# Performance work log

Measured on AMD Instinct MI355X. Metric: run time of the kernel, lower is better.

## Reference

```python
import jax, jax.numpy as jnp
import numpy as np

N_NODES = 50000
N_EDGES = 600000
D = 128
H = 128


def setup_inputs() -> dict:
    key = jax.random.key(0)
    k1, k2, k3, k4 = jax.random.split(key, 4)
    x = jax.random.normal(k1, (N_NODES, D), dtype=jnp.float32)
    edge_index = jax.random.randint(k2, (2, N_EDGES), 0, N_NODES, dtype=jnp.int64)
    # Glorot-ish init for the two linear layers of SAGEConv
    scale = 1.0 / np.sqrt(D)
    W_l = jax.random.normal(k3, (H, D), dtype=jnp.float32) * scale
    b_l = jnp.zeros((H,), dtype=jnp.float32)
    W_r = jax.random.normal(k4, (H, D), dtype=jnp.float32) * scale
    return {"x": x, "edge_index": edge_index, "W_l": W_l, "b_l": b_l, "W_r": W_r}


def reference(x, edge_index, W_l, b_l, W_r):
    # PyG SAGEConv (aggr='mean', root_weight=True):
    #   out[i] = lin_l( mean_{j->i} x[j] ) + lin_r( x[i] )
    # edge_index[0] = source nodes (j), edge_index[1] = destination nodes (i)
    src = edge_index[0]
    dst = edge_index[1]
    n = x.shape[0]
    msgs = x[src]  # [E, D] gather
    agg_sum = jax.ops.segment_sum(msgs, dst, num_segments=n)  # [N, D]
    deg = jax.ops.segment_sum(jnp.ones((src.shape[0],), dtype=x.dtype), dst, num_segments=n)
    agg = agg_sum / jnp.maximum(deg, 1.0)[:, None]  # mean aggregation; 0 for isolated nodes
    out = agg @ W_l.T + b_l + x @ W_r.T  # [N, H]
    return out
```

## Files before the change

kernel.cpp:

```cpp
#include <hip/hip_runtime.h>
#include <hip/hip_bf16.h>

using f32x4 = __attribute__((ext_vector_type(4))) float;
using s16x8 = __attribute__((ext_vector_type(8))) short;

static __device__ __forceinline__ float bflo2f(unsigned int w) {
    union { unsigned int u; float f; } c; c.u = w << 16; return c.f;
}
static __device__ __forceinline__ float bfhi2f(unsigned int w) {
    union { unsigned int u; float f; } c; c.u = w & 0xffff0000u; return c.f;
}
static __device__ __forceinline__ unsigned int f2bf(float f) {
    union { float f; unsigned int u; } c; c.f = f;
    unsigned int u = c.u;
    u = u + 0x7fffu + ((u >> 16) & 1u);
    return u >> 16;
}

#define ET 8

__global__ __launch_bounds__(256) void k_convert(
        const float* __restrict__ x, unsigned short* __restrict__ xb,
        const float* __restrict__ Wr, const float* __restrict__ Wl,
        s16x8* __restrict__ wprep, int* __restrict__ bcnt, int* __restrict__ ovfn,
        int n4, int nxb)
{
    int b = blockIdx.x;
    if (b < nxb) {
        int t = b * 256 + threadIdx.x;
        if (t >= n4) return;
        float4 v = ((const float4*)x)[t];
        ushort4 o;
        o.x = (unsigned short)f2bf(v.x);
        o.y = (unsigned short)f2bf(v.y);
        o.z = (unsigned short)f2bf(v.z);
        o.w = (unsigned short)f2bf(v.w);
        ((ushort4*)xb)[t] = o;
    } else if (b < nxb + 16) {
        int s = (b - nxb) * 256 + threadIdx.x;
        if (s >= 4096) return;
        int f = s >> 6, il = s & 63;
        int nt = f >> 3, ks = f & 7;
        int col = nt * 16 + (il & 15);
        int k   = ks * 32 + (il >> 4) * 8;
        const float* Wsrc = (k < 128) ? Wr : Wl;
        int k0 = k & 127;
        const float4* wp = (const float4*)(Wsrc + (size_t)col * 128 + k0);
        float4 w0 = wp[0], w1 = wp[1];
        s16x8 v;
        v[0] = (short)f2bf(w0.x); v[1] = (short)f2bf(w0.y);
        v[2] = (short)f2bf(w0.z); v[3] = (short)f2bf(w0.w);
        v[4] = (short)f2bf(w1.x); v[5] = (short)f2bf(w1.y);
        v[6] = (short)f2bf(w1.z); v[7] = (short)f2bf(w1.w);
        wprep[s] = v;
    } else {
        int t = threadIdx.x;
        bcnt[t] = 0;
        if (t == 0) *ovfn = 0;
    }
}

__global__ __launch_bounds__(256) void k_bin(
        const int* __restrict__ src, const int* __restrict__ dst,
        int* __restrict__ bcnt, unsigned int* __restrict__ binbuf,
        int* __restrict__ ovfn, int* __restrict__ ovf,
        int E, int NB, int capb)
{
    __shared__ int hist[256];
    __shared__ int base[256];
    int t = threadIdx.x;
    hist[t] = 0;
    __syncthreads();
    int e0 = blockIdx.x * (256 * ET);
    int bins[ET], pls[ET];
    unsigned int pay[ET];
    #pragma unroll
    for (int i = 0; i < ET; ++i) {
        int e = e0 + t + i * 256;
        bins[i] = -1;
        if (e < E) {
            int d = dst[e];
            int s = src[e];
            bins[i] = d >> 8;
            pay[i]  = ((unsigned int)(d & 255) << 24) | (unsigned int)s;
            pls[i]  = atomicAdd(&hist[bins[i]], 1);
        }
    }
    __syncthreads();
    if (t < NB && hist[t] > 0) base[t] = atomicAdd(&bcnt[t], hist[t]);
    __syncthreads();
    #pragma unroll
    for (int i = 0; i < ET; ++i) {
        if (bins[i] >= 0) {
            int pos = base[bins[i]] + pls[i];
            if (pos < capb) {
                binbuf[(size_t)bins[i] * capb + pos] = pay[i];
            } else {
                int q = atomicAdd(ovfn, 1);
                ovf[2 * q]     = (bins[i] << 8) | (int)(pay[i] >> 24);
                ovf[2 * q + 1] = (int)(pay[i] & 0xFFFFFFu);
            }
        }
    }
}

__global__ __launch_bounds__(256) void k_sort(
        const int* __restrict__ bcnt, const unsigned int* __restrict__ binbuf,
        int* __restrict__ srcS, int* __restrict__ offg, int* __restrict__ degg,
        int N, int capb)
{
    __shared__ int cnt[256];
    __shared__ int sh[256];
    __shared__ int cur[256];
    int b = blockIdx.x, t = threadIdx.x;
    int m = min(bcnt[b], capb);
    cnt[t] = 0;
    __syncthreads();
    const unsigned int* bb = binbuf + (size_t)b * capb;
    for (int j = t; j < m; j += 256)
        atomicAdd(&cnt[bb[j] >> 24], 1);
    __syncthreads();
    int v = cnt[t];
    sh[t] = v;
    __syncthreads();
    #pragma unroll
    for (int d2 = 1; d2 < 256; d2 <<= 1) {
        int y = (t >= d2) ? sh[t - d2] : 0;
        __syncthreads();
        sh[t] += y;
        __syncthreads();
    }
    int off = sh[t] - v;
    cur[t] = off;
    int node = b * 256 + t;
    if (node < N) {
        offg[node] = b * capb + off;
        degg[node] = v;
    }
    __syncthreads();
    for (int j = t; j < m; j += 256) {
        unsigned int c = bb[j];
        int p = atomicAdd(&cur[c >> 24], 1);
        srcS[(size_t)b * capb + p] = (int)(c & 0xFFFFFFu);
    }
}

__global__ __launch_bounds__(256) void k_gather_wide(
        const uint4* __restrict__ xq, const int* __restrict__ srcS,
        const int* __restrict__ offg, const int* __restrict__ degg,
        const int* __restrict__ ovfn, const int* __restrict__ ovf,
        uint4* __restrict__ abq, int N)
{
    int d    = blockIdx.x * 4 + (threadIdx.x >> 6);
    int lane = threadIdx.x & 63;
    if (d >= N) return;
    int n0 = offg[d];
    int m0 = degg[d];
    const int* sl = srcS + n0;
    int c = lane & 15, r = lane >> 4;
    float a0=0,a1=0,a2=0,a3=0,a4=0,a5=0,a6=0,a7=0;
    const uint4 z4 = {0u, 0u, 0u, 0u};
    for (int p = 0; p < m0; p += 16) {
        int pe0 = p + r, pe1 = p + 4 + r, pe2 = p + 8 + r, pe3 = p + 12 + r;
        uint4 v0 = z4, v1 = z4, v2 = z4, v3 = z4;
        if (pe0 < m0) v0 = xq[(size_t)sl[pe0] * 16 + c];
        if (pe1 < m0) v1 = xq[(size_t)sl[pe1] * 16 + c];
        if (pe2 < m0) v2 = xq[(size_t)sl[pe2] * 16 + c];
        if (pe3 < m0) v3 = xq[(size_t)sl[pe3] * 16 + c];
        a0 += bflo2f(v0.x); a1 += bfhi2f(v0.x);
        a2 += bflo2f(v0.y); a3 += bfhi2f(v0.y);
        a4 += bflo2f(v0.z); a5 += bfhi2f(v0.z);
        a6 += bflo2f(v0.w); a7 += bfhi2f(v0.w);
        a0 += bflo2f(v1.x); a1 += bfhi2f(v1.x);
        a2 += bflo2f(v1.y); a3 += bfhi2f(v1.y);
        a4 += bflo2f(v1.z); a5 += bfhi2f(v1.z);
        a6 += bflo2f(v1.w); a7 += bfhi2f(v1.w);
        a0 += bflo2f(v2.x); a1 += bfhi2f(v2.x);
        a2 += bflo2f(v2.y); a3 += bfhi2f(v2.y);
        a4 += bflo2f(v2.z); a5 += bfhi2f(v2.z);
        a6 += bflo2f(v2.w); a7 += bfhi2f(v2.w);
        a0 += bflo2f(v3.x); a1 += bfhi2f(v3.x);
        a2 += bflo2f(v3.y); a3 += bfhi2f(v3.y);
        a4 += bflo2f(v3.z); a5 += bfhi2f(v3.z);
        a6 += bflo2f(v3.w); a7 += bfhi2f(v3.w);
    }
    int deg = m0;
    int nov = *ovfn;
    for (int k = 0; k < nov; ++k) {
        if (ovf[2 * k] == d) {
            ++deg;
            if (r == 0) {
                uint4 v = xq[(size_t)ovf[2 * k + 1] * 16 + c];
                a0 += bflo2f(v.x); a1 += bfhi2f(v.x);
                a2 += bflo2f(v.y); a3 += bfhi2f(v.y);
                a4 += bflo2f(v.z); a5 += bfhi2f(v.z);
                a6 += bflo2f(v.w); a7 += bfhi2f(v.w);
            }
        }
    }
    a0 += __shfl_xor(a0, 16, 64); a0 += __shfl_xor(a0, 32, 64);
    a1 += __shfl_xor(a1, 16, 64); a1 += __shfl_xor(a1, 32, 64);
    a2 += __shfl_xor(a2, 16, 64); a2 += __shfl_xor(a2, 32, 64);
    a3 += __shfl_xor(a3, 16, 64); a3 += __shfl_xor(a3, 32, 64);
    a4 += __shfl_xor(a4, 16, 64); a4 += __shfl_xor(a4, 32, 64);
    a5 += __shfl_xor(a5, 16, 64); a5 += __shfl_xor(a5, 32, 64);
    a6 += __shfl_xor(a6, 16, 64); a6 += __shfl_xor(a6, 32, 64);
    a7 += __shfl_xor(a7, 16, 64); a7 += __shfl_xor(a7, 32, 64);
    if (r == 0) {
        float inv = 1.0f / (float)max(deg, 1);
        uint4 o;
        o.x = f2bf(a0 * inv) | (f2bf(a1 * inv) << 16);
        o.y = f2bf(a2 * inv) | (f2bf(a3 * inv) << 16);
        o.z = f2bf(a4 * inv) | (f2bf(a5 * inv) << 16);
        o.w = f2bf(a6 * inv) | (f2bf(a7 * inv) << 16);
        abq[(size_t)d * 16 + c] = o;
    }
}

__global__ __launch_bounds__(256) void k_combine_mfma(
        const unsigned short* __restrict__ xb, const unsigned short* __restrict__ ab,
        const s16x8* __restrict__ wprep,
        const float* __restrict__ bl,
        float* __restrict__ out, int N, int T)
{
    __shared__ s16x8 Bf[64][64];
    int t = threadIdx.x;
    {
        const uint4* ws = (const uint4*)wprep;
        uint4* bd = (uint4*)&Bf[0][0];
        for (int s = t; s < 4096; s += 256) bd[s] = ws[s];
    }
    __syncthreads();

    int wid = t >> 6, l = t & 63;
    int lr = l & 15, lg = l >> 4;
    float bias[8];
    #pragma unroll
    for (int nt = 0; nt < 8; ++nt) bias[nt] = bl[nt * 16 + lr];

    for (int tile = blockIdx.x; tile < T; tile += gridDim.x) {
        int rb0 = tile * 128 + wid * 32;
        int rb1 = rb0 + 16;
        int ar0 = min(rb0 + lr, N - 1);
        int ar1 = min(rb1 + lr, N - 1);
        const s16x8* xr0 = (const s16x8*)(xb + (size_t)ar0 * 128);
        const s16x8* ag0 = (const s16x8*)(ab + (size_t)ar0 * 128);
        const s16x8* xr1 = (const s16x8*)(xb + (size_t)ar1 * 128);
        const s16x8* ag1 = (const s16x8*)(ab + (size_t)ar1 * 128);
        s16x8 af0[8], af1[8];
        #pragma unroll
        for (int ks = 0; ks < 4; ++ks) {
            af0[ks]     = xr0[ks * 4 + lg];
            af0[4 + ks] = ag0[ks * 4 + lg];
            af1[ks]     = xr1[ks * 4 + lg];
            af1[4 + ks] = ag1[ks * 4 + lg];
        }

        f32x4 acc0[8], acc1[8];
        #pragma unroll
        for (int nt = 0; nt < 8; ++nt) {
            float b = bias[nt];
            acc0[nt] = (f32x4){b, b, b, b};
            acc1[nt] = (f32x4){b, b, b, b};
        }

        #pragma unroll
        for (int ks = 0; ks < 8; ++ks)
            #pragma unroll
            for (int nt = 0; nt < 8; ++nt) {
                s16x8 bfrag = Bf[nt * 8 + ks][l];
                acc0[nt] = __builtin_amdgcn_mfma_f32_16x16x32_bf16(
                               af0[ks], bfrag, acc0[nt], 0, 0, 0);
                acc1[nt] = __builtin_amdgcn_mfma_f32_16x16x32_bf16(
                               af1[ks], bfrag, acc1[nt], 0, 0, 0);
            }

        #pragma unroll
        for (int i = 0; i < 4; ++i) {
            int row0 = rb0 + lg * 4 + i;
            if (row0 < N) {
                float* op = out + (size_t)row0 * 128 + lr;
                #pragma unroll
                for (int nt = 0; nt < 8; ++nt) op[nt * 16] = acc0[nt][i];
            }
            int row1 = rb1 + lg * 4 + i;
            if (row1 < N) {
                float* op = out + (size_t)row1 * 128 + lr;
                #pragma unroll
                for (int nt = 0; nt < 8; ++nt) op[nt * 16] = acc1[nt][i];
            }
        }
    }
}


__global__ __launch_bounds__(256) void k_scatter_legacy(
        const float* __restrict__ x,
        const int* __restrict__ src, const int* __restrict__ dst,
        float* __restrict__ agg, float* __restrict__ deg, int E)
{
    int e    = (int)((blockIdx.x * 256u + threadIdx.x) >> 6);
    int lane = threadIdx.x & 63;
    if (e >= E) return;
    int s = src[e];
    int d = dst[e];
    float2 v = ((const float2*)(x + (size_t)s * 128u))[lane];
    float* ar = agg + (size_t)d * 128u;
    unsafeAtomicAdd(ar + 2 * lane,     v.x);
    unsafeAtomicAdd(ar + 2 * lane + 1, v.y);
    if (lane == 0) unsafeAtomicAdd(deg + d, 1.0f);
}

__global__ __launch_bounds__(256) void k_combine_legacy(
        const float* __restrict__ x, const float* agg, const float* __restrict__ deg,
        const float* __restrict__ Wr, const float* __restrict__ Wl,
        const float* __restrict__ bl,
        float* out, int N)
{
    __shared__ uint4 WT4[64][64];
    for (int idx = threadIdx.x; idx < 64 * 64; idx += 256) {
        int g = idx >> 6, l = idx & 63;
        uint4 wv;
        unsigned int* wp = &wv.x;
        #pragma unroll
        for (int kk = 0; kk < 4; ++kk) {
            int k = g * 4 + kk;
            const float* Wsrc = (k < 128) ? Wr : Wl;
            int km = k & 127;
            unsigned int lo = f2bf(Wsrc[(size_t)l * 128 + km]);
            unsigned int hi = f2bf(Wsrc[(size_t)(l + 64) * 128 + km]);
            wp[kk] = lo | (hi << 16);
        }
        WT4[g][l] = wv;
    }
    __syncthreads();

    int wid = threadIdx.x >> 6, lane = threadIdx.x & 63;
    float b0 = bl[lane], b1 = bl[lane + 64];
    for (int row = blockIdx.x * 4 + wid; row < N; row += gridDim.x * 4) {
        const float4* xr = (const float4*)(x   + (size_t)row * 128);
        const float4* ar = (const float4*)(agg + (size_t)row * 128);
        float inv = 1.0f / fmaxf(deg[row], 1.0f);
        float acc0 = b0, acc1 = b1;
        #pragma unroll 8
        for (int c = 0; c < 32; ++c) {
            uint4 w4 = WT4[c][lane];
            float4 q = xr[c];
            #pragma unroll
            for (int j = 0; j < 4; ++j) {
                unsigned int w = (&w4.x)[j];
                float f = (&q.x)[j];
                acc0 = fmaf(f, bflo2f(w), acc0);
                acc1 = fmaf(f, bfhi2f(w), acc1);
            }
        }
        #pragma unroll 8
        for (int c = 0; c < 32; ++c) {
            uint4 w4 = WT4[c + 32][lane];
            float4 q = ar[c];
            #pragma unroll
            for (int j = 0; j < 4; ++j) {
                unsigned int w = (&w4.x)[j];
                float f = (&q.x)[j] * inv;
                acc0 = fmaf(f, bflo2f(w), acc0);
                acc1 = fmaf(f, bfhi2f(w), acc1);
            }
        }
        out[(size_t)row * 128 + lane]      = acc0;
        out[(size_t)row * 128 + lane + 64] = acc1;
    }
}


extern "C" void kernel_launch(void* const* d_in, const int* in_sizes, int n_in,
                              void* d_out, int out_size, void* d_ws, size_t ws_size,
                              hipStream_t stream)
{
    const float* x  = (const float*)d_in[0];
    const int*   ei = (const int*)d_in[1];
    const float* Wl = (const float*)d_in[2];
    const float* bl = (const float*)d_in[3];
    const float* Wr = (const float*)d_in[4];
    float*      out = (float*)d_out;

    int N = in_sizes[0] / 128;
    int E = in_sizes[1] / 2;
    const int* src = ei;
    const int* dst = ei + E;

    int NB   = (N + 255) >> 8;
    int capb = ((2 * E / (NB > 0 ? NB : 1)) + 255) & ~255;
    size_t bfB = (size_t)N * 128 * 2;

    size_t nInts = 256 + 64 + 2 * (size_t)E + 2 * (size_t)NB * capb
                 + 2 * (size_t)N;
    size_t intsB = ((nInts * 4) + 255) & ~(size_t)255;

    if (ws_size >= intsB + 2 * bfB + 65536 && NB <= 256 && N < (1 << 24)) {
        int* bcnt = (int*)d_ws;
        int* ovfn = bcnt + 256;
        int* ovf  = ovfn + 64;
        unsigned int* binbuf = (unsigned int*)(ovf + 2 * (size_t)E);
        int* srcS = (int*)(binbuf + (size_t)NB * capb);
        int* offg = srcS + (size_t)NB * capb;
        int* degg = offg + N;
        unsigned short* xb = (unsigned short*)((char*)d_ws + intsB);
        unsigned short* ab = xb + (size_t)N * 128;
        s16x8* wprep = (s16x8*)((char*)ab + bfB);

        int nxb = (N * 32 + 255) / 256;
        int ncv = nxb + 16 + 1;
        int nbin = (E + 256 * ET - 1) / (256 * ET);

        k_convert<<<ncv, 256, 0, stream>>>(x, xb, Wr, Wl, wprep, bcnt, ovfn,
                                           N * 32, nxb);
        k_bin    <<<nbin, 256, 0, stream>>>(src, dst, bcnt, binbuf, ovfn, ovf,
                                            E, NB, capb);
        k_sort   <<<NB, 256, 0, stream>>>(bcnt, binbuf, srcS, offg, degg,
                                          N, capb);
        k_gather_wide<<<(N + 3) / 4, 256, 0, stream>>>(
                (const uint4*)xb, srcS, offg, degg, ovfn, ovf, (uint4*)ab, N);
        int T = (N + 127) / 128;
        k_combine_mfma<<<T, 256, 0, stream>>>(xb, ab, wprep, bl, out, N, T);
    } else {
        float* agg = out;
        float* deg = (float*)d_ws;
        hipMemsetAsync(out, 0, (size_t)N * 128 * 4, stream);
        hipMemsetAsync(deg, 0, (size_t)N * 4, stream);
        k_scatter_legacy<<<(E + 3) / 4, 256, 0, stream>>>(x, src, dst, agg, deg, E);
        k_combine_legacy<<<1024, 256, 0, stream>>>(x, agg, deg, Wr, Wl, bl, out, N);
    }
}
```

Baseline: 83.66 us.

## Fuse binning into convert kernel with per-block window slots, dropping global atomics

Folds the edge binning into the conversion kernel, cutting one launch. Each binning block now writes into its own fixed-size window per destination bin, with a per-block spill area, so the global atomic bucket counters and the global overflow list are gone. The sort kernel walks the per-(bin, block) windows serially, one thread per source block, and the gather kernel no longer scans an overflow list. The serial per-thread loops in the sort may be slower than the strided loop they replace. Positions are clamped to the capacity, which could silently drop edges on skewed inputs.

```diff
diff --git a/kernel.cpp b/kernel.cpp
--- a/kernel.cpp
+++ b/kernel.cpp
@@ -17,13 +17,18 @@
     return u >> 16;
 }
 
-#define ET 8
-
-__global__ __launch_bounds__(256) void k_convert(
+#define ET   16
+#define WIN  128
+#define SPB  4096
+
+__global__ __launch_bounds__(256) void k_fused(
         const float* __restrict__ x, unsigned short* __restrict__ xb,
         const float* __restrict__ Wr, const float* __restrict__ Wl,
-        s16x8* __restrict__ wprep, int* __restrict__ bcnt, int* __restrict__ ovfn,
-        int n4, int nxb)
+        s16x8* __restrict__ wprep,
+        const int* __restrict__ srcp, const int* __restrict__ dstp,
+        int* __restrict__ wincnt, unsigned int* __restrict__ binbuf,
+        int* __restrict__ spillcnt, int* __restrict__ spill,
+        int E, int n4, int nxb, int nbin, int NB)
 {
     int b = blockIdx.x;
     if (b < nxb) {
@@ -54,101 +59,108 @@
         v[6] = (short)f2bf(w1.z); v[7] = (short)f2bf(w1.w);
         wprep[s] = v;
     } else {
+        __shared__ int hist[256];
+        __shared__ int scnt;
+        int bb = b - nxb - 16;
         int t = threadIdx.x;
-        bcnt[t] = 0;
-        if (t == 0) *ovfn = 0;
-    }
-}
-
-__global__ __launch_bounds__(256) void k_bin(
-        const int* __restrict__ src, const int* __restrict__ dst,
-        int* __restrict__ bcnt, unsigned int* __restrict__ binbuf,
-        int* __restrict__ ovfn, int* __restrict__ ovf,
-        int E, int NB, int capb)
-{
-    __shared__ int hist[256];
-    __shared__ int base[256];
-    int t = threadIdx.x;
-    hist[t] = 0;
-    __syncthreads();
-    int e0 = blockIdx.x * (256 * ET);
-    int bins[ET], pls[ET];
-    unsigned int pay[ET];
-    #pragma unroll
-    for (int i = 0; i < ET; ++i) {
-        int e = e0 + t + i * 256;
-        bins[i] = -1;
-        if (e < E) {
-            int d = dst[e];
-            int s = src[e];
-            bins[i] = d >> 8;
-            pay[i]  = ((unsigned int)(d & 255) << 24) | (unsigned int)s;
-            pls[i]  = atomicAdd(&hist[bins[i]], 1);
-        }
-    }
-    __syncthreads();
-    if (t < NB && hist[t] > 0) base[t] = atomicAdd(&bcnt[t], hist[t]);
-    __syncthreads();
-    #pragma unroll
-    for (int i = 0; i < ET; ++i) {
-        if (bins[i] >= 0) {
-            int pos = base[bins[i]] + pls[i];
-            if (pos < capb) {
-                binbuf[(size_t)bins[i] * capb + pos] = pay[i];
-            } else {
-                int q = atomicAdd(ovfn, 1);
-                ovf[2 * q]     = (bins[i] << 8) | (int)(pay[i] >> 24);
-                ovf[2 * q + 1] = (int)(pay[i] & 0xFFFFFFu);
-            }
-        }
+        hist[t] = 0;
+        if (t == 0) scnt = 0;
+        __syncthreads();
+        int e0 = bb * (256 * ET);
+        int binv[ET]; unsigned int pay[ET]; int pls[ET];
+        #pragma unroll
+        for (int i = 0; i < ET; ++i) {
+            int e = e0 + t + i * 256;
+            binv[i] = -1;
+            if (e < E) {
+                int d = dstp[e];
+                binv[i] = d >> 8;
+                pay[i]  = ((unsigned int)(d & 255) << 24) | (unsigned int)srcp[e];
+                pls[i]  = atomicAdd(&hist[binv[i]], 1);
+            }
+        }
+        __syncthreads();
+        if (t < NB) wincnt[(size_t)t * nbin + bb] = min(hist[t], WIN);
+        #pragma unroll
+        for (int i = 0; i < ET; ++i) {
+            if (binv[i] >= 0) {
+                if (pls[i] < WIN) {
+                    binbuf[((size_t)binv[i] * nbin + bb) * WIN + pls[i]] = pay[i];
+                } else {
+                    int q = atomicAdd(&scnt, 1);
+                    spill[(size_t)bb * 2 * SPB + 2 * q]     = (binv[i] << 8) | (int)(pay[i] >> 24);
+                    spill[(size_t)bb * 2 * SPB + 2 * q + 1] = (int)(pay[i] & 0xFFFFFFu);
+                }
+            }
+        }
+        __syncthreads();
+        if (t == 0) spillcnt[bb] = scnt;
     }
 }
 
 __global__ __launch_bounds__(256) void k_sort(
-        const int* __restrict__ bcnt, const unsigned int* __restrict__ binbuf,
+        const int* __restrict__ wincnt, const unsigned int* __restrict__ binbuf,
+        const int* __restrict__ spillcnt, const int* __restrict__ spill,
         int* __restrict__ srcS, int* __restrict__ offg, int* __restrict__ degg,
-        int N, int capb)
+        int N, int nbin, int caps)
 {
     __shared__ int cnt[256];
-    __shared__ int sh[256];
+    __shared__ int csh[256];
     __shared__ int cur[256];
     int b = blockIdx.x, t = threadIdx.x;
-    int m = min(bcnt[b], capb);
     cnt[t] = 0;
     __syncthreads();
-    const unsigned int* bb = binbuf + (size_t)b * capb;
-    for (int j = t; j < m; j += 256)
-        atomicAdd(&cnt[bb[j] >> 24], 1);
+    int myc = 0;
+    const unsigned int* wp = nullptr;
+    if (t < nbin) {
+        myc = wincnt[(size_t)b * nbin + t];
+        wp  = binbuf + ((size_t)b * nbin + t) * WIN;
+        for (int j = 0; j < myc; ++j) atomicAdd(&cnt[wp[j] >> 24], 1);
+        int sc = spillcnt[t];
+        for (int j = 0; j < sc; ++j) {
+            int d = spill[(size_t)t * 2 * SPB + 2 * j];
+            if ((d >> 8) == b) atomicAdd(&cnt[d & 255], 1);
+        }
+    }
     __syncthreads();
     int v = cnt[t];
-    sh[t] = v;
+    csh[t] = v;
     __syncthreads();
     #pragma unroll
     for (int d2 = 1; d2 < 256; d2 <<= 1) {
-        int y = (t >= d2) ? sh[t - d2] : 0;
+        int y = (t >= d2) ? csh[t - d2] : 0;
         __syncthreads();
-        sh[t] += y;
+        csh[t] += y;
         __syncthreads();
     }
-    int off = sh[t] - v;
+    int off = csh[t] - v;
     cur[t] = off;
     int node = b * 256 + t;
     if (node < N) {
-        offg[node] = b * capb + off;
+        offg[node] = b * caps + off;
         degg[node] = v;
     }
     __syncthreads();
-    for (int j = t; j < m; j += 256) {
-        unsigned int c = bb[j];
-        int p = atomicAdd(&cur[c >> 24], 1);
-        srcS[(size_t)b * capb + p] = (int)(c & 0xFFFFFFu);
+    if (t < nbin) {
+        for (int j = 0; j < myc; ++j) {
+            unsigned int p4 = wp[j];
+            int p = min(atomicAdd(&cur[p4 >> 24], 1), caps - 1);
+            srcS[(size_t)b * caps + p] = (int)(p4 & 0xFFFFFFu);
+        }
+        int sc = spillcnt[t];
+        for (int j = 0; j < sc; ++j) {
+            int d = spill[(size_t)t * 2 * SPB + 2 * j];
+            if ((d >> 8) == b) {
+                int p = min(atomicAdd(&cur[d & 255], 1), caps - 1);
+                srcS[(size_t)b * caps + p] = spill[(size_t)t * 2 * SPB + 2 * j + 1];
+            }
+        }
     }
 }
 
 __global__ __launch_bounds__(256) void k_gather_wide(
         const uint4* __restrict__ xq, const int* __restrict__ srcS,
         const int* __restrict__ offg, const int* __restrict__ degg,
-        const int* __restrict__ ovfn, const int* __restrict__ ovf,
         uint4* __restrict__ abq, int N)
 {
     int d    = blockIdx.x * 4 + (threadIdx.x >> 6);
@@ -184,20 +196,6 @@
         a4 += bflo2f(v3.z); a5 += bfhi2f(v3.z);
         a6 += bflo2f(v3.w); a7 += bfhi2f(v3.w);
     }
-    int deg = m0;
-    int nov = *ovfn;
-    for (int k = 0; k < nov; ++k) {
-        if (ovf[2 * k] == d) {
-            ++deg;
-            if (r == 0) {
-                uint4 v = xq[(size_t)ovf[2 * k + 1] * 16 + c];
-                a0 += bflo2f(v.x); a1 += bfhi2f(v.x);
-                a2 += bflo2f(v.y); a3 += bfhi2f(v.y);
-                a4 += bflo2f(v.z); a5 += bfhi2f(v.z);
-                a6 += bflo2f(v.w); a7 += bfhi2f(v.w);
-            }
-        }
-    }
     a0 += __shfl_xor(a0, 16, 64); a0 += __shfl_xor(a0, 32, 64);
     a1 += __shfl_xor(a1, 16, 64); a1 += __shfl_xor(a1, 32, 64);
     a2 += __shfl_xor(a2, 16, 64); a2 += __shfl_xor(a2, 32, 64);
@@ -207,7 +205,7 @@
     a6 += __shfl_xor(a6, 16, 64); a6 += __shfl_xor(a6, 32, 64);
     a7 += __shfl_xor(a7, 16, 64); a7 += __shfl_xor(a7, 32, 64);
     if (r == 0) {
-        float inv = 1.0f / (float)max(deg, 1);
+        float inv = 1.0f / (float)max(m0, 1);
         uint4 o;
         o.x = f2bf(a0 * inv) | (f2bf(a1 * inv) << 16);
         o.y = f2bf(a2 * inv) | (f2bf(a3 * inv) << 16);
@@ -389,37 +387,37 @@
     const int* dst = ei + E;
 
     int NB   = (N + 255) >> 8;
-    int capb = ((2 * E / (NB > 0 ? NB : 1)) + 255) & ~255;
+    int nbin = (E + 256 * ET - 1) / (256 * ET);
+    int caps = nbin * WIN + SPB;
     size_t bfB = (size_t)N * 128 * 2;
 
-    size_t nInts = 256 + 64 + 2 * (size_t)E + 2 * (size_t)NB * capb
-                 + 2 * (size_t)N;
+    size_t nInts = 256 * (size_t)nbin + (size_t)NB * nbin * WIN + nbin
+                 + (size_t)nbin * 2 * SPB + (size_t)NB * caps + 2 * (size_t)N;
     size_t intsB = ((nInts * 4) + 255) & ~(size_t)255;
 
-    if (ws_size >= intsB + 2 * bfB + 65536 && NB <= 256 && N < (1 << 24)) {
-        int* bcnt = (int*)d_ws;
-        int* ovfn = bcnt + 256;
-        int* ovf  = ovfn + 64;
-        unsigned int* binbuf = (unsigned int*)(ovf + 2 * (size_t)E);
-        int* srcS = (int*)(binbuf + (size_t)NB * capb);
-        int* offg = srcS + (size_t)NB * capb;
-        int* degg = offg + N;
+    if (ws_size >= intsB + 2 * bfB + 65536 && NB <= 256 && nbin <= 256
+        && N < (1 << 24)) {
+        int* wincnt   = (int*)d_ws;
+        unsigned int* binbuf = (unsigned int*)(wincnt + 256 * (size_t)nbin);
+        int* spillcnt = (int*)(binbuf + (size_t)NB * nbin * WIN);
+        int* spill    = spillcnt + nbin;
+        int* srcS     = spill + (size_t)nbin * 2 * SPB;
+        int* offg     = srcS + (size_t)NB * caps;
+        int* degg     = offg + N;
         unsigned short* xb = (unsigned short*)((char*)d_ws + intsB);
         unsigned short* ab = xb + (size_t)N * 128;
         s16x8* wprep = (s16x8*)((char*)ab + bfB);
 
         int nxb = (N * 32 + 255) / 256;
-        int ncv = nxb + 16 + 1;
-        int nbin = (E + 256 * ET - 1) / (256 * ET);
-
-        k_convert<<<ncv, 256, 0, stream>>>(x, xb, Wr, Wl, wprep, bcnt, ovfn,
-                                           N * 32, nxb);
-        k_bin    <<<nbin, 256, 0, stream>>>(src, dst, bcnt, binbuf, ovfn, ovf,
-                                            E, NB, capb);
-        k_sort   <<<NB, 256, 0, stream>>>(bcnt, binbuf, srcS, offg, degg,
-                                          N, capb);
+        int ntot = nxb + 16 + nbin;
+
+        k_fused<<<ntot, 256, 0, stream>>>(x, xb, Wr, Wl, wprep, src, dst,
+                                          wincnt, binbuf, spillcnt, spill,
+                                          E, N * 32, nxb, nbin, NB);
+        k_sort <<<NB, 256, 0, stream>>>(wincnt, binbuf, spillcnt, spill,
+                                        srcS, offg, degg, N, nbin, caps);
         k_gather_wide<<<(N + 3) / 4, 256, 0, stream>>>(
-                (const uint4*)xb, srcS, offg, degg, ovfn, ovf, (uint4*)ab, N);
+                (const uint4*)xb, srcS, offg, degg, (uint4*)ab, N);
         int T = (N + 127) / 128;
         k_combine_mfma<<<T, 256, 0, stream>>>(xb, ab, wprep, bl, out, N, T);
     } else {
```

After: 88.28 us. 5.5% more time.
